# Kernel optimization log

Measured on AMD Instinct MI355X. Metric: run time of the kernel, lower is better.

The kernel has to match this reference:

```python
import jax, jax.numpy as jnp
import numpy as np

EPS = 1e-6


def setup_inputs() -> dict:
    key = jax.random.key(0)
    ks = jax.random.split(key, 5)
    B, NH, S, DQK, DV = 2, 8, 1024, 256, 512
    return {
        "q": jax.random.normal(ks[0], (B, NH, S, DQK), dtype=jnp.float32),
        "k": jax.random.normal(ks[1], (B, NH, S, DQK), dtype=jnp.float32),
        "v": jax.random.normal(ks[2], (B, NH, S, DV), dtype=jnp.float32),
        "i_preact": jax.random.normal(ks[3], (B, NH, S), dtype=jnp.float32),
        "f_preact": jax.random.normal(ks[4], (B, NH, S), dtype=jnp.float32),
    }


def reference(q, k, v, i_preact, f_preact):
    B, NH, S, DQK = q.shape
    DV = v.shape[-1]
    inv_sqrt_d = jnp.asarray(1.0 / np.sqrt(DQK), dtype=q.dtype)
    eps = jnp.asarray(EPS, dtype=q.dtype)

    C0 = jnp.zeros((B, NH, DQK, DV), dtype=q.dtype)
    n0 = jnp.zeros((B, NH, DQK), dtype=q.dtype)
    m0 = jnp.zeros((B, NH), dtype=q.dtype)

    def step(carry, xs):
        C, n, m = carry
        q_t, k_t, v_t, i_t, f_t = xs  # [B,NH,DQK],[B,NH,DQK],[B,NH,DV],[B,NH],[B,NH]
        # f_log = -log(1 + exp(-f)) = log_sigmoid(f)
        f_log = jax.nn.log_sigmoid(f_t)
        m_new = jnp.maximum(f_log + m, i_t)
        f_gate = jnp.exp(f_log + m - m_new)
        i_gate = jnp.exp(i_t - m_new)
        kv_outer = k_t[..., :, None] * v_t[..., None, :]  # [B,NH,DQK,DV]
        C = f_gate[..., None, None] * C + i_gate[..., None, None] * kv_outer
        n = f_gate[..., None] * n + i_gate[..., None] * k_t
        q_scaled = q_t * inv_sqrt_d
        h_num = jnp.einsum("bhdv,bhd->bhv", C, q_scaled)
        qn_dot = jnp.sum(n * q_scaled, axis=-1, keepdims=True)  # [B,NH,1]
        h_den = jnp.maximum(jnp.abs(qn_dot), jnp.exp(-m_new)[..., None]) + eps
        h_t = h_num / h_den
        return (C, n, m_new), h_t

    # time-major scan over S
    xs = (
        jnp.moveaxis(q, 2, 0),
        jnp.moveaxis(k, 2, 0),
        jnp.moveaxis(v, 2, 0),
        jnp.moveaxis(i_preact, 2, 0),
        jnp.moveaxis(f_preact, 2, 0),
    )
    (C, n, m), h_tm = jax.lax.scan(step, (C0, n0, m0), xs)
    h = jnp.moveaxis(h_tm, 0, 2)  # [B,NH,S,DV]
    return h, C, n, m
```

## Files before the change

kernel.cpp:

```cpp
#include <hip/hip_runtime.h>
#include <math.h>

#define SEQ   1024
#define DQ    256
#define DVD   512
#define NHH   16
#define EPSF  1e-6f
#define INV_SQRT_D 0.0625f

typedef __attribute__((ext_vector_type(8)))  short short8v;
typedef __attribute__((ext_vector_type(16))) float f32x16;

#define WS_FG    0
#define WS_IG    (NHH*SEQ)
#define WS_ELIM  (2*NHH*SEQ)
#define WS_HDEN  (3*NHH*SEQ)
#define WS_AT    (4*NHH*SEQ)
#define WS_CS    (5*NHH*SEQ)
#define WS_AC    (6*NHH*SEQ)
#define WS_BVEC  (WS_AC + NHH*16)
#define WS_SMALL_FLOATS (WS_BVEC + NHH*16*DQ)

#define QBF_OFF  ((size_t)WS_SMALL_FLOATS * 4)
#define KBF_OFF  (QBF_OFF + (size_t)NHH*SEQ*DQ*2)
#define VTB_OFF  (KBF_OFF + (size_t)NHH*SEQ*DQ*2)
#define KUT_OFF  (VTB_OFF + (size_t)NHH*DVD*SEQ*2)

__device__ __forceinline__ unsigned short f2bf(float f) {
  unsigned int u = __float_as_uint(f);
  return (unsigned short)((u + 0x7fffu + ((u >> 16) & 1u)) >> 16);
}

__device__ __forceinline__ void gl_lds16(const void* g, void* l) {
  __builtin_amdgcn_global_load_lds(
      (const __attribute__((address_space(1))) unsigned int*)g,
      (__attribute__((address_space(3))) unsigned int*)l, 16, 0, 0);
}

__global__ __launch_bounds__(256) void prep_kernel(
    const float* __restrict__ kin, const float* __restrict__ vin,
    const float* __restrict__ ipre, const float* __restrict__ fpre,
    float* __restrict__ ws,
    unsigned short* __restrict__ k_bf, unsigned short* __restrict__ vt_bf,
    unsigned short* __restrict__ kut, float* __restrict__ m_out) {
  __shared__ float lk[64][257];
  __shared__ float swsum[4], swmax[4];
  __shared__ float bndF[16], bndM[16], fin2[2];
  __shared__ float cfg[64], cig[64], cut[64];

  const int b = blockIdx.x;
  if (b < 256) {
    const int hh = b >> 4, c = b & 15;
    const int d = threadIdx.x;
    const int lane = d & 63, wid = d >> 6;
    const int tbase = hh*SEQ + c*64;
    const size_t base = (size_t)tbase * DQ;

    #pragma unroll 4
    for (int tt = 0; tt < 64; ++tt) {
      const float val = kin[base + (size_t)tt*DQ + d];
      lk[tt][d] = val;
      k_bf[base + (size_t)tt*DQ + d] = f2bf(val);
    }

    const float4 f4 = *(const float4*)(fpre + hh*SEQ + 4*d);
    const float4 i4 = *(const float4*)(ipre + hh*SEQ + 4*d);
    float fv[4] = {f4.x, f4.y, f4.z, f4.w};
    float iv[4] = {i4.x, i4.y, i4.z, i4.w};
    float fl[4], F[4];
    float s = 0.f;
    #pragma unroll
    for (int j = 0; j < 4; ++j) {
      fl[j] = fminf(fv[j], 0.f) - log1pf(expf(-fabsf(fv[j])));
      s += fl[j]; F[j] = s;
    }
    float wsc = s;
    #pragma unroll
    for (int off = 1; off < 64; off <<= 1) {
      float o = __shfl_up(wsc, off, 64);
      if (lane >= off) wsc += o;
    }
    if (lane == 63) swsum[wid] = wsc;
    __syncthreads();
    float woff = 0.f;
    #pragma unroll
    for (int i = 0; i < 4; ++i) { float t = swsum[i]; if (i < wid) woff += t; }
    const float Fexc = woff + (wsc - s);
    #pragma unroll
    for (int j = 0; j < 4; ++j) F[j] += Fexc;

    float zser[4];
    float zs = -INFINITY;
    #pragma unroll
    for (int j = 0; j < 4; ++j) {
      zs = fmaxf(zs, iv[j] - F[j]); zser[j] = zs;
    }
    float zmI = zs;
    #pragma unroll
    for (int off = 1; off < 64; off <<= 1) {
      float o = __shfl_up(zmI, off, 64);
      if (lane >= off) zmI = fmaxf(zmI, o);
    }
    if (lane == 63) swmax[wid] = zmI;
    float zexcl = __shfl_up(zmI, 1, 64);
    if (lane == 0) zexcl = -INFINITY;
    __syncthreads();
    float zoffW = -INFINITY;
    #pragma unroll
    for (int i = 0; i < 4; ++i) { float t = swmax[i]; if (i < wid) zoffW = fmaxf(zoffW, t); }
    const float zPexc = fmaxf(zoffW, zexcl);

    float mprev = Fexc + fmaxf(zPexc, 0.f);
    float m_[4], fg_[4], ig_[4];
    #pragma unroll
    for (int j = 0; j < 4; ++j) {
      const float zP = fmaxf(zPexc, zser[j]);
      m_[j] = F[j] + fmaxf(zP, 0.f);
      fg_[j] = expf(fl[j] + mprev - m_[j]);
      ig_[j] = expf(iv[j] - m_[j]);
      mprev = m_[j];
    }

    if ((d & 15) == 15) { bndF[d >> 4] = F[3]; bndM[d >> 4] = m_[3]; }
    if (d == 255)       { fin2[0] = F[3]; fin2[1] = m_[3]; }
    const int q0 = d - 16*c;
    if (q0 >= 0 && q0 < 16) {
      #pragma unroll
      for (int j = 0; j < 4; ++j) { cfg[q0*4 + j] = fg_[j]; cig[q0*4 + j] = ig_[j]; }
    }
    if (c == 0) {
      float4 o;
      o.x=fg_[0]; o.y=fg_[1]; o.z=fg_[2]; o.w=fg_[3];
      *(float4*)(ws + WS_FG + hh*SEQ + 4*d) = o;
      o.x=ig_[0]; o.y=ig_[1]; o.z=ig_[2]; o.w=ig_[3];
      *(float4*)(ws + WS_IG + hh*SEQ + 4*d) = o;
      o.x=expf(-m_[0]); o.y=expf(-m_[1]); o.z=expf(-m_[2]); o.w=expf(-m_[3]);
      *(float4*)(ws + WS_ELIM + hh*SEQ + 4*d) = o;
      o.x=F[0]-m_[0]; o.y=F[1]-m_[1]; o.z=F[2]-m_[2]; o.w=F[3]-m_[3];
      *(float4*)(ws + WS_AT + hh*SEQ + 4*d) = o;
      o.x=iv[0]-F[0]; o.y=iv[1]-F[1]; o.z=iv[2]-F[2]; o.w=iv[3]-F[3];
      *(float4*)(ws + WS_CS + hh*SEQ + 4*d) = o;
      if (d == 255) m_out[hh] = m_[3];
    }
    __syncthreads();
    if (c == 0 && d < 16) {
      const float Fp = d ? bndF[d-1] : 0.f;
      const float mp = d ? bndM[d-1] : 0.f;
      ws[WS_AC + hh*16 + d] = expf((bndF[d] - Fp) + (mp - bndM[d]));
    }
    if (q0 >= 0 && q0 < 16) {
      const float Fe = fin2[0], me = fin2[1];
      #pragma unroll
      for (int j = 0; j < 4; ++j)
        cut[q0*4 + j] = expf(Fe - F[j] + iv[j] - me);
    }
    __syncthreads();

    float nb = 0.f;
    #pragma unroll 8
    for (int tt = 0; tt < 64; ++tt) nb = cfg[tt]*nb + cig[tt]*lk[tt][d];
    ws[WS_BVEC + (hh*16 + c)*DQ + d] = nb;
    #pragma unroll
    for (int g = 0; g < 8; ++g) {
      short8v pk;
      #pragma unroll
      for (int j = 0; j < 8; ++j) {
        const int tt = g*8 + j;
        pk[j] = (short)f2bf(cut[tt] * lk[tt][d]);
      }
      *(short8v*)(kut + ((size_t)(hh*DQ + d))*SEQ + c*64 + g*8) = pk;
    }
  } else {
    const int b2 = b - 256;
    const int hh = b2 >> 5, tg = b2 & 31;
    const int tx = threadIdx.x & 31, ty = threadIdx.x >> 5;
    float (*tile)[33] = (float(*)[33])lk;
    for (int vt = 0; vt < 16; ++vt) {
      #pragma unroll
      for (int i = 0; i < 4; ++i)
        tile[ty + 8*i][tx] =
            vin[((size_t)(hh*SEQ + tg*32 + ty + 8*i))*DVD + vt*32 + tx];
      __syncthreads();
      #pragma unroll
      for (int i = 0; i < 4; ++i)
        vt_bf[((size_t)(hh*DVD + vt*32 + ty + 8*i))*SEQ + tg*32 + tx] =
            f2bf(tile[tx][ty + 8*i]);
      __syncthreads();
    }
  }
}

__global__ __launch_bounds__(256) void aux_kernel(
    const float* __restrict__ kin, const float* __restrict__ qin,
    float* __restrict__ ws, unsigned short* __restrict__ q_bf,
    float* __restrict__ n_out,
    const unsigned short* __restrict__ kut,
    const unsigned short* __restrict__ vt,
    float* __restrict__ C_out) {
  __shared__ __align__(16) char smem[66560];
  const int b = blockIdx.x;

  if (b < 256) {
    float (*pbuf)[DQ] = (float(*)[DQ])smem;
    float (*spart)[4] = (float(*)[4])(smem + 65536);
    const int hh = b >> 4;
    const int c  = b & 15;
    const int d  = threadIdx.x;

    float n = 0.f;
    for (int j = 0; j < c; ++j)
      n = ws[WS_AC + hh*16 + j]*n + ws[WS_BVEC + (hh*16 + j)*DQ + d];
    if (c == 15) {
      const float nf = ws[WS_AC + hh*16 + 15]*n +
                       ws[WS_BVEC + (hh*16 + 15)*DQ + d];
      n_out[hh*DQ + d] = nf;
    }

    const int tbase = hh*SEQ + c*64;
    const size_t base = (size_t)tbase * DQ;
    #pragma unroll 4
    for (int tt = 0; tt < 64; ++tt) {
      const float fg = ws[WS_FG + tbase + tt];
      const float ig = ws[WS_IG + tbase + tt];
      n = fg*n + ig*kin[base + (size_t)tt*DQ + d];
      const float qv = qin[base + (size_t)tt*DQ + d];
      q_bf[base + (size_t)tt*DQ + d] = f2bf(qv * INV_SQRT_D);
      pbuf[tt][d] = n * qv;
    }
    __syncthreads();

    {
      const int tt = d >> 2, qd = d & 3;
      float s = 0.f;
      #pragma unroll 8
      for (int j = 0; j < 64; ++j)
        s += pbuf[tt][qd*64 + ((j + d) & 63)];
      spart[tt][qd] = s;
    }
    __syncthreads();
    if (d < 64) {
      const float tot = (spart[d][0] + spart[d][1]) + (spart[d][2] + spart[d][3]);
      const float qn = tot * INV_SQRT_D;
      const float hd = fmaxf(fabsf(qn), ws[WS_ELIM + tbase + d]) + EPSF;
      ws[WS_HDEN + tbase + d] = hd;
    }
  } else {
    unsigned short* Alds = (unsigned short*)smem;
    unsigned short* Blds = (unsigned short*)(smem + 16384);
    const int b2 = b - 256;
    const int hh = b2 >> 4;
    const int mt = (b2 >> 3) & 1;
    const int nt = b2 & 7;
    const int tid = threadIdx.x;
    const int w = tid >> 6, lane = tid & 63, l31 = lane & 31, hl = lane >> 5;
    const int mr = w >> 1;
    const int nc = w & 1;

    f32x16 acc0 = {}, acc1 = {};
    for (int c = 0; c < 16; ++c) {
      const int t0 = c*64;
      #pragma unroll
      for (int p = 0; p < 4; ++p) {
        int u = p*256 + tid; int row = u >> 3, slot = u & 7;
        const unsigned short* src = kut +
            ((size_t)(hh*DQ + mt*128 + row))*SEQ + t0 + ((slot ^ (row & 7))*8);
        gl_lds16(src, (char*)Alds + (p*4 + w)*1024);
      }
      #pragma unroll
      for (int p = 0; p < 2; ++p) {
        int u = p*256 + tid; int row = u >> 3, slot = u & 7;
        const unsigned short* src = vt +
            ((size_t)(hh*DVD + nt*64 + row))*SEQ + t0 + ((slot ^ (row & 7))*8);
        gl_lds16(src, (char*)Blds + (p*4 + w)*1024);
      }
      __syncthreads();
      #pragma unroll
      for (int ks = 0; ks < 4; ++ks) {
        const int br = nc*32 + l31;
        short8v bf_ = *(const short8v*)&Blds[br*64 + (((ks*2 + hl) ^ (br & 7))*8)];
        const int ar0 = mr*64 + l31, ar1 = ar0 + 32;
        short8v a0 = *(const short8v*)&Alds[ar0*64 + (((ks*2 + hl) ^ (ar0 & 7))*8)];
        short8v a1 = *(const short8v*)&Alds[ar1*64 + (((ks*2 + hl) ^ (ar1 & 7))*8)];
        acc0 = __builtin_amdgcn_mfma_f32_32x32x16_bf16(a0, bf_, acc0, 0, 0, 0);
        acc1 = __builtin_amdgcn_mfma_f32_32x32x16_bf16(a1, bf_, acc1, 0, 0, 0);
      }
      __syncthreads();
    }
    #pragma unroll
    for (int r = 0; r < 16; ++r) {
      const int dl = (r & 3) + 8*(r >> 2) + 4*hl;
      const int d0 = mt*128 + mr*64 + dl;
      const size_t ob = ((size_t)(hh*DQ + d0))*DVD + nt*64 + nc*32 + l31;
      C_out[ob]            = acc0[r];
      C_out[ob + 32*DVD]   = acc1[r];
    }
  }
}

__global__ __launch_bounds__(512, 2) void attn_kernel(
    const unsigned short* __restrict__ q_bf,
    const unsigned short* __restrict__ k_bf,
    const unsigned short* __restrict__ vt_bf,
    const float* __restrict__ ws,
    float* __restrict__ h_out) {
  const int b = blockIdx.x;
  const int phase = b >> 8;
  const int idx = b & 255;
  const int hh = idx & 15;
  const int vh = (idx >> 4) & 1;
  const int qq = idx >> 5;
  const int qi = phase ? (15 - qq) : qq;
  const int nch = (qi >> 1) + 1;

  const int tid = threadIdx.x;
  const int w = tid >> 6, lane = tid & 63, l31 = lane & 31, hl = lane >> 5;
  const int tsub = w >> 2;
  const int sblk = w & 3;
  const int vsub = w & 3;

  __shared__ unsigned short Klds[128*256];
  __shared__ unsigned short Vtlds[256*128];
  __shared__ unsigned short Plds[64*128];
  __shared__ float c_lds[128];

  const float* a_g  = ws + WS_AT;
  const float* c_g  = ws + WS_CS;
  const float* hd_g = ws + WS_HDEN;

  const int tq = qi*64 + tsub*32 + l31;
  const float a_t = a_g[hh*SEQ + tq];

  short8v qfrag[16];
  #pragma unroll
  for (int d = 0; d < 16; ++d)
    qfrag[d] = *(const short8v*)(q_bf + ((size_t)(hh*SEQ + tq))*DQ + d*16 + hl*8);

  f32x16 acc0 = {}, acc1 = {};

  auto stage = [&](int c) {
    const int s0 = c*128;
    #pragma unroll
    for (int p = 0; p < 8; ++p) {
      int u = p*512 + tid;
      int row = u >> 5, slot = u & 31;
      const unsigned short* src = k_bf +
          ((size_t)(hh*SEQ + s0 + row))*DQ + ((slot ^ (row & 31))*8);
      gl_lds16(src, (char*)Klds + (p*8 + w)*1024);
    }
    #pragma unroll
    for (int p = 0; p < 8; ++p) {
      int u = p*512 + tid;
      int row = u >> 4, slot = u & 15;
      const unsigned short* src = vt_bf +
          ((size_t)(hh*DVD + vh*256 + row))*SEQ + s0 + ((slot ^ (row & 15))*8);
      gl_lds16(src, (char*)Vtlds + (p*8 + w)*1024);
    }
    if (tid < 128) c_lds[tid] = c_g[hh*SEQ + s0 + tid];
  };

  stage(0);
  __syncthreads();

  for (int c = 0; c < nch; ++c) {
    const int s0 = c*128;
    f32x16 sacc = {};
    const int srow = sblk*32 + l31;
    #pragma unroll
    for (int d = 0; d < 16; ++d) {
      short8v af = *(const short8v*)&Klds[srow*256 + (((d*2 + hl) ^ (srow & 31))*8)];
      sacc = __builtin_amdgcn_mfma_f32_32x32x16_bf16(af, qfrag[d], sacc, 0, 0, 0);
    }
    const int prow = tsub*32 + l31;
    #pragma unroll
    for (int i = 0; i < 8; ++i) {
      const int r0 = 2*i;
      const int sl = sblk*32 + (r0 & 3) + 8*(r0 >> 2) + 4*hl;
      const int sg = s0 + sl;
      const float c0 = c_lds[sl];
      const float c1 = c_lds[sl + 1];
      const float p0 = (sg     <= tq) ? __expf(a_t + c0) * sacc[r0]     : 0.f;
      const float p1 = (sg + 1 <= tq) ? __expf(a_t + c1) * sacc[r0 + 1] : 0.f;
      unsigned int pk;
      asm volatile("v_cvt_pk_bf16_f32 %0, %1, %2" : "=v"(pk) : "v"(p0), "v"(p1));
      const int byte = sl*2;
      const int slot = byte >> 4, rem = byte & 15;
      *(unsigned int*)((char*)Plds + prow*256 + ((slot ^ (prow & 15))<<4) + rem) = pk;
    }
    __syncthreads();

    #pragma unroll
    for (int ss = 0; ss < 8; ++ss) {
      const int arow = tsub*32 + l31;
      short8v pa = *(const short8v*)&Plds[arow*128 + (((ss*2 + hl) ^ (arow & 15))*8)];
      const int vr0 = vsub*64 + l31;
      const int slotB = (ss*2 + hl) ^ (l31 & 15);
      short8v vb0 = *(const short8v*)&Vtlds[vr0*128 + slotB*8];
      short8v vb1 = *(const short8v*)&Vtlds[(vr0 + 32)*128 + slotB*8];
      acc0 = __builtin_amdgcn_mfma_f32_32x32x16_bf16(pa, vb0, acc0, 0, 0, 0);
      acc1 = __builtin_amdgcn_mfma_f32_32x32x16_bf16(pa, vb1, acc1, 0, 0, 0);
    }
    __syncthreads();
    if (c + 1 < nch) { stage(c + 1); __syncthreads(); }
  }

  #pragma unroll
  for (int r = 0; r < 16; ++r) {
    const int tl = tsub*32 + (r & 3) + 8*(r >> 2) + 4*hl;
    const int tg = qi*64 + tl;
    const float inv = 1.0f / hd_g[hh*SEQ + tg];
    const size_t ob = ((size_t)(hh*SEQ + tg))*DVD + vh*256 + vsub*64 + l31;
    h_out[ob]      = acc0[r] * inv;
    h_out[ob + 32] = acc1[r] * inv;
  }
}

extern "C" void kernel_launch(void* const* d_in, const int* in_sizes, int n_in,
                              void* d_out, int out_size, void* d_ws, size_t ws_size,
                              hipStream_t stream) {
  const float* q  = (const float*)d_in[0];
  const float* k  = (const float*)d_in[1];
  const float* v  = (const float*)d_in[2];
  const float* ip = (const float*)d_in[3];
  const float* fp = (const float*)d_in[4];

  float* h_out = (float*)d_out;
  float* C_out = h_out + (size_t)NHH*SEQ*DVD;
  float* n_out = C_out + (size_t)NHH*DQ*DVD;
  float* m_out = n_out + NHH*DQ;
  float* ws    = (float*)d_ws;

  unsigned short* q_bf  = (unsigned short*)((char*)d_ws + QBF_OFF);
  unsigned short* k_bf  = (unsigned short*)((char*)d_ws + KBF_OFF);
  unsigned short* vt_bf = (unsigned short*)((char*)d_ws + VTB_OFF);
  unsigned short* kut   = (unsigned short*)((char*)d_ws + KUT_OFF);

  prep_kernel<<<768, 256, 0, stream>>>(k, v, ip, fp, ws, k_bf, vt_bf, kut, m_out);
  aux_kernel<<<512, 256, 0, stream>>>(k, q, ws, q_bf, n_out, kut, vt_bf, C_out);
  attn_kernel<<<512, 512, 0, stream>>>(q_bf, k_bf, vt_bf, ws, h_out);
}
```

Measured before the change: 88.89 us.

## Fuse aux and attention kernels, compute denominators and q conversion in-block

Merges the aux kernel (n-state recurrence, denominator, q bf16 conversion, final C GEMM) into the attention kernel. Each attention block now recomputes its own n prefix and h denominators into LDS and converts q to bf16 directly from fp32 input. The C GEMM blocks run alongside as extra blocks in the same launch. This removes one launch, the q_bf round trip and the hden workspace. The cost is that each of the two vh blocks recomputes the n recurrence, and the C-GEMM blocks use only half of their 512 threads.

```diff
diff --git a/kernel.cpp b/kernel.cpp
--- a/kernel.cpp
+++ b/kernel.cpp
@@ -14,15 +14,13 @@
 #define WS_FG    0
 #define WS_IG    (NHH*SEQ)
 #define WS_ELIM  (2*NHH*SEQ)
-#define WS_HDEN  (3*NHH*SEQ)
-#define WS_AT    (4*NHH*SEQ)
-#define WS_CS    (5*NHH*SEQ)
-#define WS_AC    (6*NHH*SEQ)
+#define WS_AT    (3*NHH*SEQ)
+#define WS_CS    (4*NHH*SEQ)
+#define WS_AC    (5*NHH*SEQ)
 #define WS_BVEC  (WS_AC + NHH*16)
 #define WS_SMALL_FLOATS (WS_BVEC + NHH*16*DQ)
 
-#define QBF_OFF  ((size_t)WS_SMALL_FLOATS * 4)
-#define KBF_OFF  (QBF_OFF + (size_t)NHH*SEQ*DQ*2)
+#define KBF_OFF  ((size_t)WS_SMALL_FLOATS * 4)
 #define VTB_OFF  (KBF_OFF + (size_t)NHH*SEQ*DQ*2)
 #define KUT_OFF  (VTB_OFF + (size_t)NHH*DVD*SEQ*2)
 
@@ -190,227 +188,235 @@
   }
 }
 
-__global__ __launch_bounds__(256) void aux_kernel(
-    const float* __restrict__ kin, const float* __restrict__ qin,
-    float* __restrict__ ws, unsigned short* __restrict__ q_bf,
-    float* __restrict__ n_out,
-    const unsigned short* __restrict__ kut,
-    const unsigned short* __restrict__ vt,
-    float* __restrict__ C_out) {
-  __shared__ __align__(16) char smem[66560];
-  const int b = blockIdx.x;
-
-  if (b < 256) {
-    float (*pbuf)[DQ] = (float(*)[DQ])smem;
-    float (*spart)[4] = (float(*)[4])(smem + 65536);
-    const int hh = b >> 4;
-    const int c  = b & 15;
-    const int d  = threadIdx.x;
-
-    float n = 0.f;
-    for (int j = 0; j < c; ++j)
-      n = ws[WS_AC + hh*16 + j]*n + ws[WS_BVEC + (hh*16 + j)*DQ + d];
-    if (c == 15) {
-      const float nf = ws[WS_AC + hh*16 + 15]*n +
-                       ws[WS_BVEC + (hh*16 + 15)*DQ + d];
-      n_out[hh*DQ + d] = nf;
-    }
-
-    const int tbase = hh*SEQ + c*64;
-    const size_t base = (size_t)tbase * DQ;
-    #pragma unroll 4
-    for (int tt = 0; tt < 64; ++tt) {
-      const float fg = ws[WS_FG + tbase + tt];
-      const float ig = ws[WS_IG + tbase + tt];
-      n = fg*n + ig*kin[base + (size_t)tt*DQ + d];
-      const float qv = qin[base + (size_t)tt*DQ + d];
-      q_bf[base + (size_t)tt*DQ + d] = f2bf(qv * INV_SQRT_D);
-      pbuf[tt][d] = n * qv;
-    }
-    __syncthreads();
-
-    {
-      const int tt = d >> 2, qd = d & 3;
-      float s = 0.f;
-      #pragma unroll 8
-      for (int j = 0; j < 64; ++j)
-        s += pbuf[tt][qd*64 + ((j + d) & 63)];
-      spart[tt][qd] = s;
-    }
-    __syncthreads();
-    if (d < 64) {
-      const float tot = (spart[d][0] + spart[d][1]) + (spart[d][2] + spart[d][3]);
-      const float qn = tot * INV_SQRT_D;
-      const float hd = fmaxf(fabsf(qn), ws[WS_ELIM + tbase + d]) + EPSF;
-      ws[WS_HDEN + tbase + d] = hd;
-    }
-  } else {
-    unsigned short* Alds = (unsigned short*)smem;
-    unsigned short* Blds = (unsigned short*)(smem + 16384);
-    const int b2 = b - 256;
-    const int hh = b2 >> 4;
-    const int mt = (b2 >> 3) & 1;
-    const int nt = b2 & 7;
-    const int tid = threadIdx.x;
-    const int w = tid >> 6, lane = tid & 63, l31 = lane & 31, hl = lane >> 5;
-    const int mr = w >> 1;
-    const int nc = w & 1;
-
-    f32x16 acc0 = {}, acc1 = {};
-    for (int c = 0; c < 16; ++c) {
-      const int t0 = c*64;
-      #pragma unroll
-      for (int p = 0; p < 4; ++p) {
-        int u = p*256 + tid; int row = u >> 3, slot = u & 7;
-        const unsigned short* src = kut +
-            ((size_t)(hh*DQ + mt*128 + row))*SEQ + t0 + ((slot ^ (row & 7))*8);
-        gl_lds16(src, (char*)Alds + (p*4 + w)*1024);
-      }
-      #pragma unroll
-      for (int p = 0; p < 2; ++p) {
-        int u = p*256 + tid; int row = u >> 3, slot = u & 7;
-        const unsigned short* src = vt +
-            ((size_t)(hh*DVD + nt*64 + row))*SEQ + t0 + ((slot ^ (row & 7))*8);
-        gl_lds16(src, (char*)Blds + (p*4 + w)*1024);
-      }
-      __syncthreads();
-      #pragma unroll
-      for (int ks = 0; ks < 4; ++ks) {
-        const int br = nc*32 + l31;
-        short8v bf_ = *(const short8v*)&Blds[br*64 + (((ks*2 + hl) ^ (br & 7))*8)];
-        const int ar0 = mr*64 + l31, ar1 = ar0 + 32;
-        short8v a0 = *(const short8v*)&Alds[ar0*64 + (((ks*2 + hl) ^ (ar0 & 7))*8)];
-        short8v a1 = *(const short8v*)&Alds[ar1*64 + (((ks*2 + hl) ^ (ar1 & 7))*8)];
-        acc0 = __builtin_amdgcn_mfma_f32_32x32x16_bf16(a0, bf_, acc0, 0, 0, 0);
-        acc1 = __builtin_amdgcn_mfma_f32_32x32x16_bf16(a1, bf_, acc1, 0, 0, 0);
-      }
-      __syncthreads();
-    }
-    #pragma unroll
-    for (int r = 0; r < 16; ++r) {
-      const int dl = (r & 3) + 8*(r >> 2) + 4*hl;
-      const int d0 = mt*128 + mr*64 + dl;
-      const size_t ob = ((size_t)(hh*DQ + d0))*DVD + nt*64 + nc*32 + l31;
-      C_out[ob]            = acc0[r];
-      C_out[ob + 32*DVD]   = acc1[r];
-    }
-  }
-}
-
-__global__ __launch_bounds__(512, 2) void attn_kernel(
-    const unsigned short* __restrict__ q_bf,
+__global__ __launch_bounds__(512, 2) void fused_kernel(
+    const float* __restrict__ qin, const float* __restrict__ kin,
     const unsigned short* __restrict__ k_bf,
     const unsigned short* __restrict__ vt_bf,
+    const unsigned short* __restrict__ kut,
     const float* __restrict__ ws,
-    float* __restrict__ h_out) {
-  const int b = blockIdx.x;
-  const int phase = b >> 8;
-  const int idx = b & 255;
-  const int hh = idx & 15;
-  const int vh = (idx >> 4) & 1;
-  const int qq = idx >> 5;
-  const int qi = phase ? (15 - qq) : qq;
-  const int nch = (qi >> 1) + 1;
-
-  const int tid = threadIdx.x;
-  const int w = tid >> 6, lane = tid & 63, l31 = lane & 31, hl = lane >> 5;
-  const int tsub = w >> 2;
-  const int sblk = w & 3;
-  const int vsub = w & 3;
-
+    float* __restrict__ h_out, float* __restrict__ C_out,
+    float* __restrict__ n_out) {
   __shared__ unsigned short Klds[128*256];
   __shared__ unsigned short Vtlds[256*128];
   __shared__ unsigned short Plds[64*128];
   __shared__ float c_lds[128];
-
-  const float* a_g  = ws + WS_AT;
-  const float* c_g  = ws + WS_CS;
-  const float* hd_g = ws + WS_HDEN;
-
-  const int tq = qi*64 + tsub*32 + l31;
-  const float a_t = a_g[hh*SEQ + tq];
-
-  short8v qfrag[16];
-  #pragma unroll
-  for (int d = 0; d < 16; ++d)
-    qfrag[d] = *(const short8v*)(q_bf + ((size_t)(hh*SEQ + tq))*DQ + d*16 + hl*8);
-
-  f32x16 acc0 = {}, acc1 = {};
-
-  auto stage = [&](int c) {
-    const int s0 = c*128;
-    #pragma unroll
-    for (int p = 0; p < 8; ++p) {
-      int u = p*512 + tid;
-      int row = u >> 5, slot = u & 31;
-      const unsigned short* src = k_bf +
-          ((size_t)(hh*SEQ + s0 + row))*DQ + ((slot ^ (row & 31))*8);
-      gl_lds16(src, (char*)Klds + (p*8 + w)*1024);
-    }
-    #pragma unroll
-    for (int p = 0; p < 8; ++p) {
-      int u = p*512 + tid;
-      int row = u >> 4, slot = u & 15;
-      const unsigned short* src = vt_bf +
-          ((size_t)(hh*DVD + vh*256 + row))*SEQ + s0 + ((slot ^ (row & 15))*8);
-      gl_lds16(src, (char*)Vtlds + (p*8 + w)*1024);
-    }
-    if (tid < 128) c_lds[tid] = c_g[hh*SEQ + s0 + tid];
-  };
-
-  stage(0);
-  __syncthreads();
-
-  for (int c = 0; c < nch; ++c) {
-    const int s0 = c*128;
-    f32x16 sacc = {};
-    const int srow = sblk*32 + l31;
-    #pragma unroll
-    for (int d = 0; d < 16; ++d) {
-      short8v af = *(const short8v*)&Klds[srow*256 + (((d*2 + hl) ^ (srow & 31))*8)];
-      sacc = __builtin_amdgcn_mfma_f32_32x32x16_bf16(af, qfrag[d], sacc, 0, 0, 0);
-    }
-    const int prow = tsub*32 + l31;
-    #pragma unroll
-    for (int i = 0; i < 8; ++i) {
-      const int r0 = 2*i;
-      const int sl = sblk*32 + (r0 & 3) + 8*(r0 >> 2) + 4*hl;
-      const int sg = s0 + sl;
-      const float c0 = c_lds[sl];
-      const float c1 = c_lds[sl + 1];
-      const float p0 = (sg     <= tq) ? __expf(a_t + c0) * sacc[r0]     : 0.f;
-      const float p1 = (sg + 1 <= tq) ? __expf(a_t + c1) * sacc[r0 + 1] : 0.f;
-      unsigned int pk;
-      asm volatile("v_cvt_pk_bf16_f32 %0, %1, %2" : "=v"(pk) : "v"(p0), "v"(p1));
-      const int byte = sl*2;
-      const int slot = byte >> 4, rem = byte & 15;
-      *(unsigned int*)((char*)Plds + prow*256 + ((slot ^ (prow & 15))<<4) + rem) = pk;
-    }
+  __shared__ float spart[64][4];
+  __shared__ float hd_lds[64];
+
+  const int b = blockIdx.x;
+  const int tid = threadIdx.x;
+
+  if (b < 512) {
+    const int phase = b >> 8;
+    const int idx = b & 255;
+    const int hh = idx & 15;
+    const int vh = (idx >> 4) & 1;
+    const int qq = idx >> 5;
+    const int qi = phase ? (15 - qq) : qq;
+    const int nch = (qi >> 1) + 1;
+
+    const int w = tid >> 6, lane = tid & 63, l31 = lane & 31, hl = lane >> 5;
+    const int tsub = w >> 2;
+    const int sblk = w & 3;
+    const int vsub = w & 3;
+
+    const float* a_g  = ws + WS_AT;
+    const float* c_g  = ws + WS_CS;
+
+    const int tbase = hh*SEQ + qi*64;
+
+    {
+      float* pbuf = (float*)Klds;
+      if (tid < 256) {
+        const int d = tid;
+        float n = 0.f;
+        for (int j = 0; j < qi; ++j)
+          n = ws[WS_AC + hh*16 + j]*n + ws[WS_BVEC + (hh*16 + j)*DQ + d];
+        if (qi == 15 && vh == 0) {
+          const float nf = ws[WS_AC + hh*16 + 15]*n +
+                           ws[WS_BVEC + (hh*16 + 15)*DQ + d];
+          n_out[hh*DQ + d] = nf;
+        }
+        const size_t base = (size_t)tbase * DQ;
+        #pragma unroll 4
+        for (int tt = 0; tt < 64; ++tt) {
+          const float fg = ws[WS_FG + tbase + tt];
+          const float ig = ws[WS_IG + tbase + tt];
+          n = fg*n + ig*kin[base + (size_t)tt*DQ + d];
+          pbuf[tt*256 + d] = n * qin[base + (size_t)tt*DQ + d];
+        }
+      }
+      __syncthreads();
+      if (tid < 256) {
+        const int d = tid;
+        const int tt = d >> 2, qd = d & 3;
+        float s = 0.f;
+        #pragma unroll 8
+        for (int j = 0; j < 64; ++j)
+          s += pbuf[tt*256 + qd*64 + ((j + d) & 63)];
+        spart[tt][qd] = s;
+      }
+      __syncthreads();
+      if (tid < 64) {
+        const float tot = (spart[tid][0] + spart[tid][1]) +
+                          (spart[tid][2] + spart[tid][3]);
+        const float qn = tot * INV_SQRT_D;
+        hd_lds[tid] = fmaxf(fabsf(qn), ws[WS_ELIM + tbase + tid]) + EPSF;
+      }
+      __syncthreads();
+    }
+
+    const int tq = qi*64 + tsub*32 + l31;
+    const float a_t = a_g[hh*SEQ + tq];
+
+    short8v qfrag[16];
+    {
+      const float* qrow = qin + (size_t)(hh*SEQ + tq)*DQ;
+      #pragma unroll
+      for (int d2 = 0; d2 < 16; ++d2) {
+        const float4 a = *(const float4*)(qrow + d2*16 + hl*8);
+        const float4 bq = *(const float4*)(qrow + d2*16 + hl*8 + 4);
+        short8v f;
+        f[0]=(short)f2bf(a.x*INV_SQRT_D);  f[1]=(short)f2bf(a.y*INV_SQRT_D);
+        f[2]=(short)f2bf(a.z*INV_SQRT_D);  f[3]=(short)f2bf(a.w*INV_SQRT_D);
+        f[4]=(short)f2bf(bq.x*INV_SQRT_D); f[5]=(short)f2bf(bq.y*INV_SQRT_D);
+        f[6]=(short)f2bf(bq.z*INV_SQRT_D); f[7]=(short)f2bf(bq.w*INV_SQRT_D);
+        qfrag[d2] = f;
+      }
+    }
+
+    f32x16 acc0 = {}, acc1 = {};
+
+    auto stage = [&](int c) {
+      const int s0 = c*128;
+      #pragma unroll
+      for (int p = 0; p < 8; ++p) {
+        int u = p*512 + tid;
+        int row = u >> 5, slot = u & 31;
+        const unsigned short* src = k_bf +
+            ((size_t)(hh*SEQ + s0 + row))*DQ + ((slot ^ (row & 31))*8);
+        gl_lds16(src, (char*)Klds + (p*8 + w)*1024);
+      }
+      #pragma unroll
+      for (int p = 0; p < 8; ++p) {
+        int u = p*512 + tid;
+        int row = u >> 4, slot = u & 15;
+        const unsigned short* src = vt_bf +
+            ((size_t)(hh*DVD + vh*256 + row))*SEQ + s0 + ((slot ^ (row & 15))*8);
+        gl_lds16(src, (char*)Vtlds + (p*8 + w)*1024);
+      }
+      if (tid < 128) c_lds[tid] = c_g[hh*SEQ + s0 + tid];
+    };
+
+    stage(0);
     __syncthreads();
 
-    #pragma unroll
-    for (int ss = 0; ss < 8; ++ss) {
-      const int arow = tsub*32 + l31;
-      short8v pa = *(const short8v*)&Plds[arow*128 + (((ss*2 + hl) ^ (arow & 15))*8)];
-      const int vr0 = vsub*64 + l31;
-      const int slotB = (ss*2 + hl) ^ (l31 & 15);
-      short8v vb0 = *(const short8v*)&Vtlds[vr0*128 + slotB*8];
-      short8v vb1 = *(const short8v*)&Vtlds[(vr0 + 32)*128 + slotB*8];
-      acc0 = __builtin_amdgcn_mfma_f32_32x32x16_bf16(pa, vb0, acc0, 0, 0, 0);
-      acc1 = __builtin_amdgcn_mfma_f32_32x32x16_bf16(pa, vb1, acc1, 0, 0, 0);
-    }
-    __syncthreads();
-    if (c + 1 < nch) { stage(c + 1); __syncthreads(); }
-  }
-
-  #pragma unroll
-  for (int r = 0; r < 16; ++r) {
-    const int tl = tsub*32 + (r & 3) + 8*(r >> 2) + 4*hl;
-    const int tg = qi*64 + tl;
-    const float inv = 1.0f / hd_g[hh*SEQ + tg];
-    const size_t ob = ((size_t)(hh*SEQ + tg))*DVD + vh*256 + vsub*64 + l31;
-    h_out[ob]      = acc0[r] * inv;
-    h_out[ob + 32] = acc1[r] * inv;
+    for (int c = 0; c < nch; ++c) {
+      const int s0 = c*128;
+      f32x16 sacc = {};
+      const int srow = sblk*32 + l31;
+      #pragma unroll
+      for (int d = 0; d < 16; ++d) {
+        short8v af = *(const short8v*)&Klds[srow*256 + (((d*2 + hl) ^ (srow & 31))*8)];
+        sacc = __builtin_amdgcn_mfma_f32_32x32x16_bf16(af, qfrag[d], sacc, 0, 0, 0);
+      }
+      const int prow = tsub*32 + l31;
+      #pragma unroll
+      for (int i = 0; i < 8; ++i) {
+        const int r0 = 2*i;
+        const int sl = sblk*32 + (r0 & 3) + 8*(r0 >> 2) + 4*hl;
+        const int sg = s0 + sl;
+        const float c0 = c_lds[sl];
+        const float c1 = c_lds[sl + 1];
+        const float p0 = (sg     <= tq) ? __expf(a_t + c0) * sacc[r0]     : 0.f;
+        const float p1 = (sg + 1 <= tq) ? __expf(a_t + c1) * sacc[r0 + 1] : 0.f;
+        unsigned int pk;
+        asm volatile("v_cvt_pk_bf16_f32 %0, %1, %2" : "=v"(pk) : "v"(p0), "v"(p1));
+        const int byte = sl*2;
+        const int slot = byte >> 4, rem = byte & 15;
+        *(unsigned int*)((char*)Plds + prow*256 + ((slot ^ (prow & 15))<<4) + rem) = pk;
+      }
+      __syncthreads();
+
+      #pragma unroll
+      for (int ss = 0; ss < 8; ++ss) {
+        const int arow = tsub*32 + l31;
+        short8v pa = *(const short8v*)&Plds[arow*128 + (((ss*2 + hl) ^ (arow & 15))*8)];
+        const int vr0 = vsub*64 + l31;
+        const int slotB = (ss*2 + hl) ^ (l31 & 15);
+        short8v vb0 = *(const short8v*)&Vtlds[vr0*128 + slotB*8];
+        short8v vb1 = *(const short8v*)&Vtlds[(vr0 + 32)*128 + slotB*8];
+        acc0 = __builtin_amdgcn_mfma_f32_32x32x16_bf16(pa, vb0, acc0, 0, 0, 0);
+        acc1 = __builtin_amdgcn_mfma_f32_32x32x16_bf16(pa, vb1, acc1, 0, 0, 0);
+      }
+      __syncthreads();
+      if (c + 1 < nch) { stage(c + 1); __syncthreads(); }
+    }
+
+    #pragma unroll
+    for (int r = 0; r < 16; ++r) {
+      const int tl = tsub*32 + (r & 3) + 8*(r >> 2) + 4*hl;
+      const int tg = qi*64 + tl;
+      const float inv = 1.0f / hd_lds[tl];
+      const size_t ob = ((size_t)(hh*SEQ + tg))*DVD + vh*256 + vsub*64 + l31;
+      h_out[ob]      = acc0[r] * inv;
+      h_out[ob + 32] = acc1[r] * inv;
+    }
+  } else {
+    unsigned short* Alds = (unsigned short*)Klds;
+    unsigned short* Blds = (unsigned short*)Vtlds;
+    const int b2 = b - 512;
+    const int hh = b2 >> 4;
+    const int mt = (b2 >> 3) & 1;
+    const int nt = b2 & 7;
+    const int w = tid >> 6, lane = tid & 63, l31 = lane & 31, hl = lane >> 5;
+    const int mr = w >> 1;
+    const int nc = w & 1;
+
+    f32x16 acc0 = {}, acc1 = {};
+    for (int c = 0; c < 16; ++c) {
+      const int t0 = c*64;
+      if (tid < 256) {
+        #pragma unroll
+        for (int p = 0; p < 4; ++p) {
+          int u = p*256 + tid; int row = u >> 3, slot = u & 7;
+          const unsigned short* src = kut +
+              ((size_t)(hh*DQ + mt*128 + row))*SEQ + t0 + ((slot ^ (row & 7))*8);
+          gl_lds16(src, (char*)Alds + (p*4 + w)*1024);
+        }
+        #pragma unroll
+        for (int p = 0; p < 2; ++p) {
+          int u = p*256 + tid; int row = u >> 3, slot = u & 7;
+          const unsigned short* src = vt_bf +
+              ((size_t)(hh*DVD + nt*64 + row))*SEQ + t0 + ((slot ^ (row & 7))*8);
+          gl_lds16(src, (char*)Blds + (p*4 + w)*1024);
+        }
+      }
+      __syncthreads();
+      if (tid < 256) {
+        #pragma unroll
+        for (int ks = 0; ks < 4; ++ks) {
+          const int br = nc*32 + l31;
+          short8v bf_ = *(const short8v*)&Blds[br*64 + (((ks*2 + hl) ^ (br & 7))*8)];
+          const int ar0 = mr*64 + l31, ar1 = ar0 + 32;
+          short8v a0 = *(const short8v*)&Alds[ar0*64 + (((ks*2 + hl) ^ (ar0 & 7))*8)];
+          short8v a1 = *(const short8v*)&Alds[ar1*64 + (((ks*2 + hl) ^ (ar1 & 7))*8)];
+          acc0 = __builtin_amdgcn_mfma_f32_32x32x16_bf16(a0, bf_, acc0, 0, 0, 0);
+          acc1 = __builtin_amdgcn_mfma_f32_32x32x16_bf16(a1, bf_, acc1, 0, 0, 0);
+        }
+      }
+      __syncthreads();
+    }
+    if (tid < 256) {
+      #pragma unroll
+      for (int r = 0; r < 16; ++r) {
+        const int dl = (r & 3) + 8*(r >> 2) + 4*hl;
+        const int d0 = mt*128 + mr*64 + dl;
+        const size_t ob = ((size_t)(hh*DQ + d0))*DVD + nt*64 + nc*32 + l31;
+        C_out[ob]            = acc0[r];
+        C_out[ob + 32*DVD]   = acc1[r];
+      }
+    }
   }
 }
 
@@ -429,12 +435,11 @@
   float* m_out = n_out + NHH*DQ;
   float* ws    = (float*)d_ws;
 
-  unsigned short* q_bf  = (unsigned short*)((char*)d_ws + QBF_OFF);
   unsigned short* k_bf  = (unsigned short*)((char*)d_ws + KBF_OFF);
   unsigned short* vt_bf = (unsigned short*)((char*)d_ws + VTB_OFF);
   unsigned short* kut   = (unsigned short*)((char*)d_ws + KUT_OFF);
 
   prep_kernel<<<768, 256, 0, stream>>>(k, v, ip, fp, ws, k_bf, vt_bf, kut, m_out);
-  aux_kernel<<<512, 256, 0, stream>>>(k, q, ws, q_bf, n_out, kut, vt_bf, C_out);
-  attn_kernel<<<512, 512, 0, stream>>>(q_bf, k_bf, vt_bf, ws, h_out);
+  fused_kernel<<<768, 512, 0, stream>>>(q, k, k_bf, vt_bf, kut, ws,
+                                        h_out, C_out, n_out);
 }
```

New measurement: 126.0 us. 1.42x slower.
